# Kernel optimization log

Measured on AMD Instinct MI355X. Metric: run time of the kernel, lower is better.

The kernel has to match this reference:

```python
import jax, jax.numpy as jnp
import numpy as np

C = 256
WT_LEVELS = 3
SQ = 0.7071067811865476  # 1/sqrt(2), Haar/db1 coefficient
# Filters exactly as stored in the torch module (pywt db1, dec filters reversed):
DEC_LO = jnp.array([SQ, SQ], dtype=jnp.float32)
DEC_HI = jnp.array([SQ, -SQ], dtype=jnp.float32)
REC_LO = jnp.array([SQ, SQ], dtype=jnp.float32)
REC_HI = jnp.array([SQ, -SQ], dtype=jnp.float32)


def _conv_same(x, w, groups):
    # torch F.conv1d(padding='same'): total pad = k-1, left = total//2, rest right
    k = w.shape[-1]
    total = k - 1
    pad = (total // 2, total - total // 2)
    return jax.lax.conv_general_dilated(
        x, w, window_strides=(1,), padding=[pad],
        dimension_numbers=('NCH', 'OIH', 'NCH'),
        feature_group_count=groups)


def _dw_filter(filt, c):
    # depthwise weight [C, 1, k] from a 1D filter, matching .expand(C, -1, -1)
    return jnp.broadcast_to(filt.reshape(1, 1, -1), (c, 1, filt.shape[0]))


def _dwt(x):
    c = x.shape[1]
    lo = _conv_same(x, _dw_filter(DEC_LO, c), c)[:, :, ::2]
    hi = _conv_same(x, _dw_filter(DEC_HI, c), c)[:, :, ::2]
    return lo, hi


def _idwt(lo, hi):
    c = lo.shape[1]
    lo = jnp.repeat(lo, 2, axis=2)  # F.interpolate nearest, scale_factor=2
    hi = jnp.repeat(hi, 2, axis=2)
    lo = _conv_same(lo, _dw_filter(REC_LO, c), c)
    hi = _conv_same(hi, _dw_filter(REC_HI, c), c)
    m = min(lo.shape[2], hi.shape[2])
    return lo[:, :, :m] + hi[:, :, :m]


def setup_inputs() -> dict:
    key = jax.random.key(0)
    ks = jax.random.split(key, 7)
    B, L, K = 8, 16384, 5
    x = jax.random.normal(ks[0], (B, C, L), dtype=jnp.float32)
    conv_w = jax.random.normal(ks[1], (C, C, K), dtype=jnp.float32) * 0.05
    conv_b = jax.random.normal(ks[2], (C,), dtype=jnp.float32) * 0.05
    wconv0 = jax.random.normal(ks[3], (C, 1, K), dtype=jnp.float32) * 0.2
    wconv1 = jax.random.normal(ks[4], (C, 1, K), dtype=jnp.float32) * 0.2
    wconv2 = jax.random.normal(ks[5], (C, 1, K), dtype=jnp.float32) * 0.2
    scale = jnp.ones((1, C, 1), dtype=jnp.float32)
    return {"x": x, "conv_w": conv_w, "conv_b": conv_b,
            "wconv0": wconv0, "wconv1": wconv1, "wconv2": wconv2,
            "scale": scale}


def reference(x, conv_w, conv_b, wconv0, wconv1, wconv2, scale):
    # main full conv (groups=1, bias)
    out = _conv_same(x, conv_w, 1) + conv_b[None, :, None]

    # wavelet decomposition: dets collected finest->coarsest
    a = x
    dets = []
    for _ in range(WT_LEVELS):
        a, d = _dwt(a)
        dets.append(d)
    # coeffs[::-1] = [approx, d_coarsest, ..., d_finest];
    # wavelet_convs[i] applied in that order
    d_coarse = _conv_same(dets[2], wconv0, C)
    d_mid = _conv_same(dets[1], wconv1, C)
    d_fine = _conv_same(dets[0], wconv2, C)

    rec = _idwt(a, d_coarse)
    rec = _idwt(rec, d_mid)
    rec = _idwt(rec, d_fine)
    # L divisible by 2**WT_LEVELS -> rec length == orig length (no interpolate)

    return out + scale * rec
```

## Files before the change

kernel.cpp:

```cpp
#include <hip/hip_runtime.h>
#include <hip/hip_bf16.h>
#include <stdint.h>

#define SQF 0.70710678118654752f
#define SQ2 1.41421356237309505f

typedef __bf16 bf16x8 __attribute__((ext_vector_type(8)));
typedef float f32x4 __attribute__((ext_vector_type(4)));

using GLp = const __attribute__((address_space(1))) void*;
using LDp = __attribute__((address_space(3))) void*;

__device__ __forceinline__ unsigned short f2bf(float f) {
  union { float f; uint32_t u; } v; v.f = f;
  uint32_t r = v.u + 0x7fffu + ((v.u >> 16) & 1u);
  return (unsigned short)(r >> 16);
}

__global__ void prepack_w(const float* __restrict__ w, unsigned short* __restrict__ Wp) {
  int f = blockIdx.x * 256 + threadIdx.x;
  if (f >= 40 * 8192) return;
  int e = f & 7;
  int lane = (f >> 3) & 63;
  int cog = (f >> 9) & 15;
  int ks = f >> 13;
  int co = cog * 16 + (lane & 15);
  int ci = (ks & 7) * 32 + (lane >> 4) * 8 + e;
  int k = ks >> 3;
  Wp[f] = f2bf(w[(co * 256 + ci) * 5 + k]);
}

__global__ void transpose_x(const float* __restrict__ x, unsigned short* __restrict__ xT) {
  __shared__ __attribute__((aligned(16))) unsigned short Ts[64 * 72];
  const int lt = blockIdx.x, ct = blockIdx.y, b = blockIdx.z;
  const int t = threadIdx.x;
  const int l0 = lt * 64, ci0 = ct * 64;
#pragma unroll
  for (int p = 0; p < 4; ++p) {
    int cil = p * 16 + (t >> 4);
    int ll = (t & 15) * 4;
    const float4 v = *(const float4*)(x + (((size_t)b * 256 + ci0 + cil) * 16384 + l0 + ll));
    Ts[(ll + 0) * 72 + cil] = f2bf(v.x);
    Ts[(ll + 1) * 72 + cil] = f2bf(v.y);
    Ts[(ll + 2) * 72 + cil] = f2bf(v.z);
    Ts[(ll + 3) * 72 + cil] = f2bf(v.w);
  }
  __syncthreads();
#pragma unroll
  for (int p = 0; p < 4; ++p) {
    int ll = p * 16 + (t >> 4);
    int cq = (t & 15) * 4;
    ushort4 v = *(const ushort4*)(&Ts[ll * 72 + cq]);
    *(ushort4*)(xT + (((size_t)b * 16384 + l0 + ll) * 256 + ci0 + cq)) = v;
  }
}

__global__ __launch_bounds__(512, 4)
void conv_mfma(const unsigned short* __restrict__ xT, const unsigned short* __restrict__ Wp,
               const float* __restrict__ bias, float* __restrict__ out) {
  __shared__ __attribute__((aligned(16))) unsigned short Xs[132 * 256];
  const int tid = threadIdx.x;
  const int lane = tid & 63;
  const int wv = tid >> 6;
  const int wm = wv & 3;
  const int wn = wv >> 2;
  const int lt = blockIdx.x;
  const int b = blockIdx.y;
  const int l0 = lt << 7;
  const int r15 = lane & 15, g = lane >> 4;

  if (lt == 0 && tid < 64) *(float4*)(&Xs[tid * 8]) = float4{0.f, 0.f, 0.f, 0.f};
  if (lt == 127 && tid < 64) *(float4*)(&Xs[130 * 256 + tid * 8]) = float4{0.f, 0.f, 0.f, 0.f};

  {
    const size_t xbase = (size_t)b * 16384 * 256;
#pragma unroll
    for (int it = 0; it < 9; ++it) {
      int idx = it * 512 + tid;
      if (idx >= 132 * 32) break;
      int row = idx >> 5, cl = idx & 31;
      int l = l0 - 2 + row;
      void* ldst = (void*)(Xs + ((idx & ~63) << 3));
      if (l >= 0 && l < 16384) {
        const unsigned short* src = xT + xbase + (size_t)l * 256 + ((cl ^ (row & 7)) << 3);
        __builtin_amdgcn_global_load_lds((GLp)src, (LDp)ldst, 16, 0, 0);
      }
    }
  }

  auto loadA = [&](bf16x8* a, int ks) {
#pragma unroll
    for (int mf = 0; mf < 4; ++mf)
      a[mf] = *reinterpret_cast<const bf16x8*>(
          Wp + (size_t)ks * 8192 + ((wm * 4 + mf) << 9) + (lane << 3));
  };
  auto loadB = [&](bf16x8* bv, int ks) {
    const int k = ks >> 3, cb = ks & 7;
    const int c = cb * 4 + g;
    const int jb = wn * 64 + r15 + k;
#pragma unroll
    for (int nf = 0; nf < 4; ++nf) {
      int j = jb + nf * 16;
      bv[nf] = *reinterpret_cast<const bf16x8*>(&Xs[j * 256 + ((c ^ (j & 7)) << 3)]);
    }
  };

  f32x4 acc[4][4];
#pragma unroll
  for (int mf = 0; mf < 4; ++mf)
#pragma unroll
    for (int nf = 0; nf < 4; ++nf) acc[mf][nf] = f32x4{0.f, 0.f, 0.f, 0.f};

  bf16x8 aA[4], aB[4], bfr[4];
  loadA(aA, 0);
  __syncthreads();

  for (int ks = 0; ks < 40; ks += 2) {
    loadA(aB, ks + 1);
    loadB(bfr, ks);
#pragma unroll
    for (int mf = 0; mf < 4; ++mf)
#pragma unroll
      for (int nf = 0; nf < 4; ++nf)
        acc[mf][nf] = __builtin_amdgcn_mfma_f32_16x16x32_bf16(aA[mf], bfr[nf], acc[mf][nf], 0, 0, 0);
    if (ks < 38) loadA(aA, ks + 2);
    loadB(bfr, ks + 1);
#pragma unroll
    for (int mf = 0; mf < 4; ++mf)
#pragma unroll
      for (int nf = 0; nf < 4; ++nf)
        acc[mf][nf] = __builtin_amdgcn_mfma_f32_16x16x32_bf16(aB[mf], bfr[nf], acc[mf][nf], 0, 0, 0);
  }

  const size_t ob = (size_t)b * 256 * 16384;
  const int lglob = l0 + wn * 64 + r15;
#pragma unroll
  for (int mf = 0; mf < 4; ++mf) {
    int co0 = wm * 64 + mf * 16 + g * 4;
#pragma unroll
    for (int r = 0; r < 4; ++r) {
      float bv = bias[co0 + r];
#pragma unroll
      for (int nf = 0; nf < 4; ++nf)
        out[ob + (size_t)(co0 + r) * 16384 + lglob + nf * 16] = acc[mf][nf][r] + bv;
    }
  }
}

__global__ void conv_naive(const float* __restrict__ x, const float* __restrict__ w,
                           const float* __restrict__ bias, float* __restrict__ out) {
  int l = blockIdx.x * 256 + threadIdx.x;
  int co = blockIdx.y, b = blockIdx.z;
  float acc = bias[co];
  const float* xb = x + (size_t)b * 256 * 16384;
  const float* wr = w + (size_t)co * 256 * 5;
  for (int ci = 0; ci < 256; ++ci) {
    const float* xc = xb + (size_t)ci * 16384;
    const float* wc = wr + ci * 5;
#pragma unroll
    for (int k = 0; k < 5; ++k) {
      int j = l + k - 2;
      float v = (j >= 0 && j < 16384) ? xc[j] : 0.f;
      acc += wc[k] * v;
    }
  }
  out[((size_t)b * 256 + co) * 16384 + l] = acc;
}

#define OFF_D1  0
#define OFF_D2  8192
#define OFF_R1  12288
#define OFF_A3  16384
#define OFF_D3  18432
#define OFF_R2O 16384

__device__ __forceinline__ float conv5(const float* a, const float* w, int idx, int len) {
  if (idx >= len) return 0.f;
  float s = 0.f;
#pragma unroll
  for (int t = 0; t < 5; ++t) {
    int j = idx + t - 2;
    float v = (j >= 0 && j < len) ? a[j] : 0.f;
    s += w[t] * v;
  }
  return s;
}

__global__ __launch_bounds__(512, 2)
void wavelet_add(const float* __restrict__ x, const float* __restrict__ w0g,
                 const float* __restrict__ w1g, const float* __restrict__ w2g,
                 const float* __restrict__ scale, float* __restrict__ out) {
  __shared__ __attribute__((aligned(16))) float S[20480];
  const int t = threadIdx.x;
  const int bc = blockIdx.x;
  const int c = bc & 255;
  const size_t rowbase = (size_t)bc * 16384;
  float w0[5], w1[5], w2[5];
#pragma unroll
  for (int i = 0; i < 5; ++i) { w0[i] = w0g[c * 5 + i]; w1[i] = w1g[c * 5 + i]; w2[i] = w2g[c * 5 + i]; }
  const float sc = scale[c];

  {
    const float4* x4 = (const float4*)(x + rowbase);
#pragma unroll
    for (int s = 0; s < 4; ++s) {
      int i = s * 512 + t;
      float4 u = x4[2 * i];
      float4 v = x4[2 * i + 1];
      float a10 = SQF * (u.x + u.y), d10 = SQF * (u.x - u.y);
      float a11 = SQF * (u.z + u.w), d11 = SQF * (u.z - u.w);
      float a12 = SQF * (v.x + v.y), d12 = SQF * (v.x - v.y);
      float a13 = SQF * (v.z + v.w), d13 = SQF * (v.z - v.w);
      *(float4*)(&S[OFF_D1 + 4 * i]) = float4{d10, d11, d12, d13};
      float a20 = SQF * (a10 + a11), d20 = SQF * (a10 - a11);
      float a21 = SQF * (a12 + a13), d21 = SQF * (a12 - a13);
      *(float2*)(&S[OFF_D2 + 2 * i]) = float2{d20, d21};
      S[OFF_A3 + i] = SQF * (a20 + a21);
      S[OFF_D3 + i] = SQF * (a20 - a21);
    }
  }
  __syncthreads();
  {
    const float* A3 = &S[OFF_A3]; const float* D3 = &S[OFF_D3];
#pragma unroll
    for (int s = 0; s < 4; ++s) {
      int i = s * 512 + t;
      float a3 = A3[i];
      float a3p = (i < 2047) ? A3[i + 1] : 0.f;
      float dc = conv5(D3, w0, i, 2048);
      float dcp = conv5(D3, w0, i + 1, 2048);
      *(float2*)(&S[OFF_R1 + 2 * i]) = float2{SQ2 * a3, SQF * (a3 + a3p + dc - dcp)};
    }
  }
  __syncthreads();
  {
    const float* R1 = &S[OFF_R1]; const float* D2 = &S[OFF_D2];
#pragma unroll
    for (int s = 0; s < 8; ++s) {
      int i = s * 512 + t;
      float r1 = R1[i];
      float r1p = (i < 4095) ? R1[i + 1] : 0.f;
      float dm = conv5(D2, w1, i, 4096);
      float dmp = conv5(D2, w1, i + 1, 4096);
      S[OFF_R2O + i] = SQF * (r1 + r1p + dm - dmp);
    }
  }
  __syncthreads();
  {
    const float* R1 = &S[OFF_R1]; const float* R2O = &S[OFF_R2O]; const float* D1 = &S[OFF_D1];
    float4* op = (float4*)(out + rowbase);
#pragma unroll
    for (int s = 0; s < 8; ++s) {
      int m = s * 512 + t;
      float r1 = R1[m];
      float r1p = (m < 4095) ? R1[m + 1] : 0.f;
      float ro = R2O[m];
      float e0 = SQ2 * r1;
      float e1 = SQ2 * r1p;
      float df0 = conv5(D1, w2, 2 * m, 8192);
      float df1 = conv5(D1, w2, 2 * m + 1, 8192);
      float df2 = conv5(D1, w2, 2 * m + 2, 8192);
      float4 cu = op[m];
      cu.x += sc * (SQ2 * e0);
      cu.y += sc * (SQF * (e0 + ro + df0 - df1));
      cu.z += sc * (SQ2 * ro);
      cu.w += sc * (SQF * (ro + e1 + df1 - df2));
      op[m] = cu;
    }
  }
}

extern "C" void kernel_launch(void* const* d_in, const int* in_sizes, int n_in,
                              void* d_out, int out_size, void* d_ws, size_t ws_size,
                              hipStream_t stream) {
  const float* x = (const float*)d_in[0];
  const float* conv_w = (const float*)d_in[1];
  const float* conv_b = (const float*)d_in[2];
  const float* w0 = (const float*)d_in[3];
  const float* w1 = (const float*)d_in[4];
  const float* w2 = (const float*)d_in[5];
  const float* scale = (const float*)d_in[6];
  float* out = (float*)d_out;

  const size_t XT_BYTES = 67108864ull;
  const size_t WP_BYTES = 655360ull;
  if (ws_size >= XT_BYTES + WP_BYTES) {
    unsigned short* xT = (unsigned short*)d_ws;
    unsigned short* Wp = (unsigned short*)((char*)d_ws + XT_BYTES);
    prepack_w<<<dim3(1280), dim3(256), 0, stream>>>(conv_w, Wp);
    transpose_x<<<dim3(256, 4, 8), dim3(256), 0, stream>>>(x, xT);
    conv_mfma<<<dim3(128, 8), dim3(512), 0, stream>>>(xT, Wp, conv_b, out);
  } else {
    conv_naive<<<dim3(64, 256, 8), dim3(256), 0, stream>>>(x, conv_w, conv_b, out);
  }
  wavelet_add<<<dim3(2048), dim3(512), 0, stream>>>(x, w0, w1, w2, scale, out);
}
```

Baseline: 184.5 us.

## Fuse x transpose/bf16 cast into conv tile load; store finest details as bf16

Removes the separate transpose_x kernel and its 64 MB bf16 workspace. The conv kernel now reads fp32 x directly in channel-major order, converts it to bf16 and writes the swizzled LDS tile itself, dropping the async global_load_lds path. The wavelet kernel keeps the finest detail band in LDS as bf16, shrinking shared memory, which may raise occupancy. In exchange, conv loads become strided scalar fp32 reads, the tile load is no longer asynchronous, and the finest-band convolution loses some precision.

```diff
diff --git a/kernel.cpp b/kernel.cpp
--- a/kernel.cpp
+++ b/kernel.cpp
@@ -7,14 +7,14 @@
 
 typedef __bf16 bf16x8 __attribute__((ext_vector_type(8)));
 typedef float f32x4 __attribute__((ext_vector_type(4)));
-
-using GLp = const __attribute__((address_space(1))) void*;
-using LDp = __attribute__((address_space(3))) void*;
 
 __device__ __forceinline__ unsigned short f2bf(float f) {
   union { float f; uint32_t u; } v; v.f = f;
   uint32_t r = v.u + 0x7fffu + ((v.u >> 16) & 1u);
   return (unsigned short)(r >> 16);
+}
+__device__ __forceinline__ float bf2f(unsigned short h) {
+  union { uint32_t u; float f; } v; v.u = (uint32_t)h << 16; return v.f;
 }
 
 __global__ void prepack_w(const float* __restrict__ w, unsigned short* __restrict__ Wp) {
@@ -30,33 +30,8 @@
   Wp[f] = f2bf(w[(co * 256 + ci) * 5 + k]);
 }
 
-__global__ void transpose_x(const float* __restrict__ x, unsigned short* __restrict__ xT) {
-  __shared__ __attribute__((aligned(16))) unsigned short Ts[64 * 72];
-  const int lt = blockIdx.x, ct = blockIdx.y, b = blockIdx.z;
-  const int t = threadIdx.x;
-  const int l0 = lt * 64, ci0 = ct * 64;
-#pragma unroll
-  for (int p = 0; p < 4; ++p) {
-    int cil = p * 16 + (t >> 4);
-    int ll = (t & 15) * 4;
-    const float4 v = *(const float4*)(x + (((size_t)b * 256 + ci0 + cil) * 16384 + l0 + ll));
-    Ts[(ll + 0) * 72 + cil] = f2bf(v.x);
-    Ts[(ll + 1) * 72 + cil] = f2bf(v.y);
-    Ts[(ll + 2) * 72 + cil] = f2bf(v.z);
-    Ts[(ll + 3) * 72 + cil] = f2bf(v.w);
-  }
-  __syncthreads();
-#pragma unroll
-  for (int p = 0; p < 4; ++p) {
-    int ll = p * 16 + (t >> 4);
-    int cq = (t & 15) * 4;
-    ushort4 v = *(const ushort4*)(&Ts[ll * 72 + cq]);
-    *(ushort4*)(xT + (((size_t)b * 16384 + l0 + ll) * 256 + ci0 + cq)) = v;
-  }
-}
-
 __global__ __launch_bounds__(512, 4)
-void conv_mfma(const unsigned short* __restrict__ xT, const unsigned short* __restrict__ Wp,
+void conv_mfma(const float* __restrict__ x, const unsigned short* __restrict__ Wp,
                const float* __restrict__ bias, float* __restrict__ out) {
   __shared__ __attribute__((aligned(16))) unsigned short Xs[132 * 256];
   const int tid = threadIdx.x;
@@ -69,21 +44,32 @@
   const int l0 = lt << 7;
   const int r15 = lane & 15, g = lane >> 4;
 
-  if (lt == 0 && tid < 64) *(float4*)(&Xs[tid * 8]) = float4{0.f, 0.f, 0.f, 0.f};
-  if (lt == 127 && tid < 64) *(float4*)(&Xs[130 * 256 + tid * 8]) = float4{0.f, 0.f, 0.f, 0.f};
-
-  {
-    const size_t xbase = (size_t)b * 16384 * 256;
-#pragma unroll
-    for (int it = 0; it < 9; ++it) {
-      int idx = it * 512 + tid;
-      if (idx >= 132 * 32) break;
-      int row = idx >> 5, cl = idx & 31;
-      int l = l0 - 2 + row;
-      void* ldst = (void*)(Xs + ((idx & ~63) << 3));
-      if (l >= 0 && l < 16384) {
-        const unsigned short* src = xT + xbase + (size_t)l * 256 + ((cl ^ (row & 7)) << 3);
-        __builtin_amdgcn_global_load_lds((GLp)src, (LDp)ldst, 16, 0, 0);
+  {
+    const int tl = tid & 127;
+    const int cg = tid >> 7;
+    const float* xb = x + (size_t)b * 256 * 16384;
+#pragma unroll
+    for (int rep = 0; rep < 2; ++rep) {
+      int j = rep * 128 + tl;
+      if (j >= 132) break;
+      int l = l0 - 2 + j;
+      bool inb = (l >= 0 && l < 16384);
+      const float* xl = xb + l;
+#pragma unroll
+      for (int i8 = 0; i8 < 16; ++i8) {
+        int ci = cg * 64 + i8 * 4;
+        float v0 = 0.f, v1 = 0.f, v2 = 0.f, v3 = 0.f;
+        if (inb) {
+          v0 = xl[(size_t)(ci + 0) * 16384];
+          v1 = xl[(size_t)(ci + 1) * 16384];
+          v2 = xl[(size_t)(ci + 2) * 16384];
+          v3 = xl[(size_t)(ci + 3) * 16384];
+        }
+        uint32_t p0 = ((uint32_t)f2bf(v1) << 16) | f2bf(v0);
+        uint32_t p1 = ((uint32_t)f2bf(v3) << 16) | f2bf(v2);
+        int slot = (ci >> 3) ^ (j & 7);
+        int byteoff = j * 512 + (slot << 4) + (ci & 7) * 2;
+        *(uint2*)((char*)Xs + byteoff) = uint2{p0, p1};
       }
     }
   }
@@ -167,12 +153,11 @@
   out[((size_t)b * 256 + co) * 16384 + l] = acc;
 }
 
-#define OFF_D1  0
-#define OFF_D2  8192
-#define OFF_R1  12288
-#define OFF_A3  16384
-#define OFF_D3  18432
-#define OFF_R2O 16384
+#define OFF_D2  0
+#define OFF_R1  4096
+#define OFF_A3  8192
+#define OFF_D3  10240
+#define OFF_R2O 8192
 
 __device__ __forceinline__ float conv5(const float* a, const float* w, int idx, int len) {
   if (idx >= len) return 0.f;
@@ -185,12 +170,24 @@
   }
   return s;
 }
+__device__ __forceinline__ float conv5h(const unsigned short* a, const float* w, int idx, int len) {
+  if (idx >= len) return 0.f;
+  float s = 0.f;
+#pragma unroll
+  for (int t = 0; t < 5; ++t) {
+    int j = idx + t - 2;
+    float v = (j >= 0 && j < len) ? bf2f(a[j]) : 0.f;
+    s += w[t] * v;
+  }
+  return s;
+}
 
 __global__ __launch_bounds__(512, 2)
 void wavelet_add(const float* __restrict__ x, const float* __restrict__ w0g,
                  const float* __restrict__ w1g, const float* __restrict__ w2g,
                  const float* __restrict__ scale, float* __restrict__ out) {
-  __shared__ __attribute__((aligned(16))) float S[20480];
+  __shared__ __attribute__((aligned(16))) unsigned short D1h[8192];
+  __shared__ __attribute__((aligned(16))) float S[12288];
   const int t = threadIdx.x;
   const int bc = blockIdx.x;
   const int c = bc & 255;
@@ -211,7 +208,9 @@
       float a11 = SQF * (u.z + u.w), d11 = SQF * (u.z - u.w);
       float a12 = SQF * (v.x + v.y), d12 = SQF * (v.x - v.y);
       float a13 = SQF * (v.z + v.w), d13 = SQF * (v.z - v.w);
-      *(float4*)(&S[OFF_D1 + 4 * i]) = float4{d10, d11, d12, d13};
+      uint32_t q0 = ((uint32_t)f2bf(d11) << 16) | f2bf(d10);
+      uint32_t q1 = ((uint32_t)f2bf(d13) << 16) | f2bf(d12);
+      *(uint2*)(&D1h[4 * i]) = uint2{q0, q1};
       float a20 = SQF * (a10 + a11), d20 = SQF * (a10 - a11);
       float a21 = SQF * (a12 + a13), d21 = SQF * (a12 - a13);
       *(float2*)(&S[OFF_D2 + 2 * i]) = float2{d20, d21};
@@ -247,7 +246,7 @@
   }
   __syncthreads();
   {
-    const float* R1 = &S[OFF_R1]; const float* R2O = &S[OFF_R2O]; const float* D1 = &S[OFF_D1];
+    const float* R1 = &S[OFF_R1]; const float* R2O = &S[OFF_R2O];
     float4* op = (float4*)(out + rowbase);
 #pragma unroll
     for (int s = 0; s < 8; ++s) {
@@ -257,9 +256,9 @@
       float ro = R2O[m];
       float e0 = SQ2 * r1;
       float e1 = SQ2 * r1p;
-      float df0 = conv5(D1, w2, 2 * m, 8192);
-      float df1 = conv5(D1, w2, 2 * m + 1, 8192);
-      float df2 = conv5(D1, w2, 2 * m + 2, 8192);
+      float df0 = conv5h(D1h, w2, 2 * m, 8192);
+      float df1 = conv5h(D1h, w2, 2 * m + 1, 8192);
+      float df2 = conv5h(D1h, w2, 2 * m + 2, 8192);
       float4 cu = op[m];
       cu.x += sc * (SQ2 * e0);
       cu.y += sc * (SQF * (e0 + ro + df0 - df1));
@@ -282,14 +281,11 @@
   const float* scale = (const float*)d_in[6];
   float* out = (float*)d_out;
 
-  const size_t XT_BYTES = 67108864ull;
   const size_t WP_BYTES = 655360ull;
-  if (ws_size >= XT_BYTES + WP_BYTES) {
-    unsigned short* xT = (unsigned short*)d_ws;
-    unsigned short* Wp = (unsigned short*)((char*)d_ws + XT_BYTES);
+  if (ws_size >= WP_BYTES) {
+    unsigned short* Wp = (unsigned short*)d_ws;
     prepack_w<<<dim3(1280), dim3(256), 0, stream>>>(conv_w, Wp);
-    transpose_x<<<dim3(256, 4, 8), dim3(256), 0, stream>>>(x, xT);
-    conv_mfma<<<dim3(128, 8), dim3(512), 0, stream>>>(xT, Wp, conv_b, out);
+    conv_mfma<<<dim3(128, 8), dim3(512), 0, stream>>>(x, Wp, conv_b, out);
   } else {
     conv_naive<<<dim3(64, 256, 8), dim3(256), 0, stream>>>(x, conv_w, conv_b, out);
   }
```

New measurement: 179.5 us. 2.7% less time.
